# Kernel tuning notes

Measured on AMD Instinct MI355X. Metric: run time of the kernel, lower is better.

## Reference

```python
import jax, jax.numpy as jnp
import numpy as np

NEIGHBOR_NUM = 10   # FLAGS.gcn_n_num
SUPPORT_NUM = 7     # FLAGS.gcn_sup_num


def _norm(x, axis=-1):
    # F.normalize: divide by norm clamped to 1e-12
    return x / jnp.clip(jnp.linalg.norm(x, axis=axis, keepdims=True), 1e-12)


def _knn(v, k):
    # pairwise squared-distance KNN, excluding self -> (b, n, k)
    d2 = jnp.sum(v * v, -1)
    dist = d2[:, :, None] + d2[:, None, :] - 2.0 * jnp.einsum('bic,bjc->bij', v, v)
    idx = jax.lax.top_k(-dist, k + 1)[1]
    return idx[:, :, 1:]


_gather = jax.vmap(lambda f, i: f[i])  # f:(v,c), i:(v,k) -> (v,k,c)


def _orl(feat, w):
    # hybrid-scope fusion: concat per-point feature with global mean, 1x1 conv, residual
    g = jnp.broadcast_to(feat.mean(1, keepdims=True), feat.shape)
    return jnp.einsum('bvc,oc->bvo', jnp.concatenate([feat, g], -1), w) + feat


def _surface(verts, n, dirs, ste_w, orl_w):
    # HSlayer_surface: directional supports on normalized neighbor offsets
    b, v, _ = verts.shape
    f_ste = jnp.einsum('bvc,oc->bvo', verts, ste_w)              # (b,v,K)
    dnorm = _norm(_gather(verts, _knn(verts, n)) - verts[:, :, None, :])  # (b,v,n,3)
    theta = jax.nn.relu(jnp.einsum('bvnc,cs->bvns', dnorm, _norm(dirs, 0)))  # (b,v,n,S*K)
    theta = theta.reshape(b, v, n, SUPPORT_NUM, -1)
    return _orl(theta.max(2).sum(2) + f_ste, orl_w)


def _hs(verts, fmap, n, w, bias, dirs, ste_w, orl_w, out_c):
    # HS_layer: support-weighted aggregation of projected neighbor features
    b, v, _ = verts.shape
    f_ste = jnp.einsum('bvc,oc->bvo', fmap, ste_w)
    idx = _knn(verts, n)
    dnorm = _norm(_gather(verts, idx) - verts[:, :, None, :])
    theta = jax.nn.relu(jnp.einsum('bvnc,cs->bvns', dnorm, _norm(dirs, 0)))  # (b,v,n,S*O)
    fout = fmap @ w + bias                        # (b,v,(S+1)*O)
    f_center = fout[..., :out_c]
    f_support = _gather(fout[..., out_c:], idx)   # (b,v,n,S*O)
    act = (theta * f_support).reshape(b, v, n, SUPPORT_NUM, out_c)
    return _orl(f_center + act.max(2).sum(2) + f_ste, orl_w)


def _bn(x, g, b, eps=1e-5):
    # BatchNorm1d (training mode, biased variance) over (batch, vertices)
    m = x.mean((0, 1))
    var = ((x - m) ** 2).mean((0, 1))
    return (x - m) * jax.lax.rsqrt(var + eps) * g + b


def _pool(verts, fmap, rate=4, k=4):
    # neighborhood max-pool then deterministic 1/rate subsample
    pooled = _gather(fmap, _knn(verts, k)).max(2)
    pn = verts.shape[1] // rate
    return verts[:, :pn], pooled[:, :pn]


def setup_inputs() -> dict:
    key = jax.random.key(0)
    ks = iter(jax.random.split(key, 40))
    r = lambda *s: jax.random.normal(next(ks), s, jnp.float32) * 0.05
    S = SUPPORT_NUM
    return dict(
        vertices=jax.random.normal(next(ks), (4, 4096, 3), jnp.float32),
        dirs0=r(3, S * 128), ste0=r(128, 3), orl0=r(128, 256),
        w1=r(128, (S + 1) * 128), b1=r((S + 1) * 128), dirs1=r(3, S * 128),
        ste1=r(128, 128), orl1=r(128, 256),
        bn1_g=jnp.ones(128, jnp.float32), bn1_b=jnp.zeros(128, jnp.float32),
        w2=r(128, (S + 1) * 256), b2=r((S + 1) * 256), dirs2=r(3, S * 256),
        ste2=r(256, 128), orl2=r(256, 512),
        bn2_g=jnp.ones(256, jnp.float32), bn2_b=jnp.zeros(256, jnp.float32),
        w3=r(256, (S + 1) * 256), b3=r((S + 1) * 256), dirs3=r(3, S * 256),
        ste3=r(256, 256), orl3=r(256, 512),
        bn3_g=jnp.ones(256, jnp.float32), bn3_b=jnp.zeros(256, jnp.float32),
        w4=r(256, (S + 1) * 512), b4=r((S + 1) * 512), dirs4=r(3, S * 512),
        ste4=r(512, 256), orl4=r(512, 1024),
    )


def reference(vertices, dirs0, ste0, orl0,
              w1, b1, dirs1, ste1, orl1, bn1_g, bn1_b,
              w2, b2, dirs2, ste2, orl2, bn2_g, bn2_b,
              w3, b3, dirs3, ste3, orl3, bn3_g, bn3_b,
              w4, b4, dirs4, ste4, orl4):
    n = NEIGHBOR_NUM
    fm0 = jax.nn.relu(_surface(vertices, n, dirs0, ste0, orl0))
    fm1 = jax.nn.relu(_bn(_hs(vertices, fm0, n, w1, b1, dirs1, ste1, orl1, 128), bn1_g, bn1_b))
    v1, fp1 = _pool(vertices, fm1)
    n1 = min(n, v1.shape[1] // 8)
    fm2 = jax.nn.relu(_bn(_hs(v1, fp1, n1, w2, b2, dirs2, ste2, orl2, 256), bn2_g, bn2_b))
    fm3 = jax.nn.relu(_bn(_hs(v1, fm2, n1, w3, b3, dirs3, ste3, orl3, 256), bn3_g, bn3_b))
    v2, fp2 = _pool(v1, fm3)
    n2 = min(n, v2.shape[1] // 8)
    fm4 = _hs(v2, fp2, n2, w4, b4, dirs4, ste4, orl4, 512)
    return fm4.max(1)  # (bs, 512)
```

## Files before the change

### kernel.cpp

```cpp
#include <hip/hip_runtime.h>

#define S_NUM 7
#define NB 10
#define NEG_INF (-3.402823466e38f)


struct NormSeg { const float* src; float* dst; int M; };

__global__ void normalize_all_kernel(NormSeg s0, NormSeg s1, NormSeg s2, NormSeg s3, NormSeg s4) {
  NormSeg s;
  switch (blockIdx.y) {
    case 0: s = s0; break;
    case 1: s = s1; break;
    case 2: s = s2; break;
    case 3: s = s3; break;
    default: s = s4; break;
  }
  int m = blockIdx.x * blockDim.x + threadIdx.x;
  if (m >= s.M) return;
  float a = s.src[m], b = s.src[s.M + m], c = s.src[2 * s.M + m];
  float L = fmaxf(sqrtf(a * a + b * b + c * c), 1e-12f);
  s.dst[m] = a / L; s.dst[s.M + m] = b / L; s.dst[2 * s.M + m] = c / L;
}

struct TSeg { const float* in; float* out; int R, Cfull, Csub; };

__global__ void transpose_all_kernel(TSeg t0, TSeg t1, TSeg t2, TSeg t3, TSeg t4,
                                     TSeg t5, TSeg t6, TSeg t7, TSeg t8) {
  TSeg s;
  switch (blockIdx.y) {
    case 0: s = t0; break; case 1: s = t1; break; case 2: s = t2; break;
    case 3: s = t3; break; case 4: s = t4; break; case 5: s = t5; break;
    case 6: s = t6; break; case 7: s = t7; break; default: s = t8; break;
  }
  int t = blockIdx.x * blockDim.x + threadIdx.x;
  if (t >= s.R * s.Csub) return;
  int r = t % s.R, c = t / s.R;
  s.out[(size_t)c * s.R + r] = s.in[(size_t)r * s.Cfull + c];
}

__global__ void pack_points_kernel(const float* __restrict__ verts, float4* __restrict__ pts, int total) {
  int t = blockIdx.x * blockDim.x + threadIdx.x;
  if (t >= total) return;
  float x = verts[3 * t], y = verts[3 * t + 1], z = verts[3 * t + 2];
  float d2 = x * x + y * y + z * z;
  pts[t] = make_float4(x, y, z, d2);
}

__device__ __forceinline__ unsigned long long knn_key(float dist, int j) {
  unsigned int fb = __float_as_uint(dist);
  fb ^= ((unsigned int)((int)fb >> 31)) | 0x80000000u;
  return ((unsigned long long)fb << 32) | (unsigned int)j;
}

template <int V>
__global__ __launch_bounds__(256) void knn_kernel(const float4* __restrict__ pts,
                                                  int* __restrict__ idx_out) {
  constexpr int ITERS = V / 64;
  constexpr int FILL = (ITERS < 11) ? ITERS : 11;
  int wave = threadIdx.x >> 6;
  int lane = threadIdx.x & 63;
  int i = blockIdx.x * 4 + wave;
  int b = blockIdx.y;
  const float4* pb = pts + (size_t)b * 4096;
  float4 pi = pb[i];
  unsigned long long top[11];
#pragma unroll
  for (int t = 0; t < 11; ++t) top[t] = ~0ull;
  const float4* pl = pb + lane;
#pragma unroll
  for (int t = 0; t < FILL; ++t) {
    int j = lane + t * 64;
    float4 pj = pl[t * 64];
    float dt = pi.x * pj.x + pi.y * pj.y + pi.z * pj.z;
    float dist = (pi.w + pj.w) - 2.0f * dt;
    if (j == i) dist = -1.0f;
    top[t] = knn_key(dist, j);
  }
#pragma unroll
  for (int p = 0; p < 11; ++p) {
#pragma unroll
    for (int q = (p & 1); q + 1 < 11; q += 2) {
      unsigned long long a = top[q], bb = top[q + 1];
      bool cgt = a > bb;
      top[q] = cgt ? bb : a;
      top[q + 1] = cgt ? a : bb;
    }
  }
#pragma unroll 2
  for (int t = FILL; t < ITERS; ++t) {
    int j = lane + t * 64;
    float4 pj = pl[t * 64];
    float dt = pi.x * pj.x + pi.y * pj.y + pi.z * pj.z;
    float dist = (pi.w + pj.w) - 2.0f * dt;
    if (j == i) dist = -1.0f;
    unsigned long long key = knn_key(dist, j);
    if (key < top[10]) {
      unsigned long long ck = key;
#pragma unroll
      for (int q = 0; q < 11; ++q) {
        unsigned long long a = top[q];
        bool cl = ck < a;
        top[q] = cl ? ck : a;
        ck = cl ? a : ck;
      }
    }
  }
#pragma unroll 1
  for (int t = 0; t < 11; ++t) {
    unsigned long long m = top[0];
#pragma unroll
    for (int o = 32; o > 0; o >>= 1) {
      unsigned long long other = __shfl_xor(m, o, 64);
      m = (other < m) ? other : m;
    }
    if (top[0] == m) {
#pragma unroll
      for (int q = 0; q < 10; ++q) top[q] = top[q + 1];
      top[10] = ~0ull;
    }
    if (t >= 1 && lane == 0)
      idx_out[((size_t)b * V + i) * NB + (t - 1)] = (int)(m & 0xffffffffu);
  }
}

__global__ __launch_bounds__(256) void gemm_kernel(
    const float* __restrict__ A, const float* __restrict__ B,
    const float* __restrict__ bias, const float* __restrict__ gt,
    const float* __restrict__ resid, float* __restrict__ C,
    int M, int N, int K, int rpb, int relu) {
  __shared__ float As[32][68];
  __shared__ float Bs[32][64];
  int bm = blockIdx.x * 64;
  int bn = blockIdx.y * 64;
  int tid = threadIdx.x;
  int tx = tid & 15, ty = tid >> 4;
  float acc[4][4] = {};
  for (int k0 = 0; k0 < K; k0 += 32) {
#pragma unroll
    for (int l = 0; l < 2; ++l) {
      int f = tid + l * 256;
      int row = f >> 3, kq = f & 7;
      float4 a = *reinterpret_cast<const float4*>(&A[(size_t)(bm + row) * K + k0 + kq * 4]);
      As[kq * 4 + 0][row] = a.x; As[kq * 4 + 1][row] = a.y;
      As[kq * 4 + 2][row] = a.z; As[kq * 4 + 3][row] = a.w;
    }
#pragma unroll
    for (int l = 0; l < 2; ++l) {
      int f = tid + l * 256;
      int row = f >> 4, cq = f & 15;
      float4 v = *reinterpret_cast<const float4*>(&B[(size_t)(k0 + row) * N + bn + cq * 4]);
      *reinterpret_cast<float4*>(&Bs[row][cq * 4]) = v;
    }
    __syncthreads();
#pragma unroll
    for (int kk = 0; kk < 32; ++kk) {
      float4 av = *reinterpret_cast<const float4*>(&As[kk][ty * 4]);
      float4 bv = *reinterpret_cast<const float4*>(&Bs[kk][tx * 4]);
      float am[4] = {av.x, av.y, av.z, av.w};
      float bb[4] = {bv.x, bv.y, bv.z, bv.w};
#pragma unroll
      for (int i2 = 0; i2 < 4; ++i2)
#pragma unroll
        for (int j2 = 0; j2 < 4; ++j2)
          acc[i2][j2] = fmaf(am[i2], bb[j2], acc[i2][j2]);
    }
    __syncthreads();
  }
#pragma unroll
  for (int i2 = 0; i2 < 4; ++i2) {
    int row = bm + ty * 4 + i2;
    int col0 = bn + tx * 4;
    float4 v;
    float* vv = reinterpret_cast<float*>(&v);
#pragma unroll
    for (int j2 = 0; j2 < 4; ++j2) {
      float t = acc[i2][j2];
      int col = col0 + j2;
      if (bias)  t += bias[col];
      if (resid) t += resid[(size_t)row * N + col];
      if (gt)    t += gt[(row / rpb) * N + col];
      if (relu)  t = fmaxf(t, 0.0f);
      vv[j2] = t;
    }
    *reinterpret_cast<float4*>(&C[(size_t)row * N + col0]) = v;
  }
}

__global__ __launch_bounds__(128) void surface0_kernel(const float* __restrict__ verts,
    const int* __restrict__ idx, const float* __restrict__ ndirs,
    const float* __restrict__ ste0, float* __restrict__ feat) {
  __shared__ float dn[NB][3];
  int b = blockIdx.y, v = blockIdx.x;
  const float* vb = verts + (size_t)b * 4096 * 3;
  int tid = threadIdx.x;
  if (tid < NB) {
    int j = idx[((size_t)b * 4096 + v) * NB + tid];
    float dx = vb[3 * j] - vb[3 * v];
    float dy = vb[3 * j + 1] - vb[3 * v + 1];
    float dz = vb[3 * j + 2] - vb[3 * v + 2];
    float L = fmaxf(sqrtf(dx * dx + dy * dy + dz * dz), 1e-12f);
    dn[tid][0] = dx / L; dn[tid][1] = dy / L; dn[tid][2] = dz / L;
  }
  __syncthreads();
  int c = tid;
  float acc = vb[3 * v] * ste0[c * 3] + vb[3 * v + 1] * ste0[c * 3 + 1] + vb[3 * v + 2] * ste0[c * 3 + 2];
#pragma unroll
  for (int s = 0; s < S_NUM; ++s) {
    float w0 = ndirs[s * 128 + c], w1 = ndirs[896 + s * 128 + c], w2 = ndirs[1792 + s * 128 + c];
    float mx = NEG_INF;
#pragma unroll
    for (int n = 0; n < NB; ++n) {
      float th = fmaxf(dn[n][0] * w0 + dn[n][1] * w1 + dn[n][2] * w2, 0.0f);
      mx = fmaxf(mx, th);
    }
    acc += mx;
  }
  feat[((size_t)b * 4096 + v) * 128 + c] = acc;
}

template <int C>
__global__ void hs_kernel(const float* __restrict__ verts, int V,
                          const int* __restrict__ idx, const float* __restrict__ ndirs,
                          const float* __restrict__ fout, const float* __restrict__ fste,
                          float* __restrict__ feat) {
  __shared__ float dn[NB][3];
  __shared__ int nbr[NB];
  int b = blockIdx.y, v = blockIdx.x;
  const float* vb = verts + (size_t)b * 4096 * 3;
  int tid = threadIdx.x;
  if (tid < NB) {
    int j = idx[((size_t)b * V + v) * NB + tid];
    nbr[tid] = j;
    float dx = vb[3 * j] - vb[3 * v];
    float dy = vb[3 * j + 1] - vb[3 * v + 1];
    float dz = vb[3 * j + 2] - vb[3 * v + 2];
    float L = fmaxf(sqrtf(dx * dx + dy * dy + dz * dz), 1e-12f);
    dn[tid][0] = dx / L; dn[tid][1] = dy / L; dn[tid][2] = dz / L;
  }
  __syncthreads();
  int c = tid;
  size_t row = (size_t)b * V + v;
  float w0[S_NUM], w1[S_NUM], w2[S_NUM];
#pragma unroll
  for (int s = 0; s < S_NUM; ++s) {
    w0[s] = ndirs[s * C + c];
    w1[s] = ndirs[S_NUM * C + s * C + c];
    w2[s] = ndirs[2 * S_NUM * C + s * C + c];
  }
  float mx[S_NUM];
#pragma unroll
  for (int s = 0; s < S_NUM; ++s) mx[s] = NEG_INF;
  for (int n = 0; n < NB; ++n) {
    float d0 = dn[n][0], d1 = dn[n][1], d2 = dn[n][2];
    const float* fb = fout + ((size_t)b * V + nbr[n]) * (8 * C) + C + c;
#pragma unroll
    for (int s = 0; s < S_NUM; ++s) {
      float th = fmaxf(d0 * w0[s] + d1 * w1[s] + d2 * w2[s], 0.0f);
      mx[s] = fmaxf(mx[s], th * fb[(size_t)s * C]);
    }
  }
  float acc = fout[row * (8 * C) + c] + fste[row * C + c];
#pragma unroll
  for (int s = 0; s < S_NUM; ++s) acc += mx[s];
  feat[row * C + c] = acc;
}


__global__ void colsum_kernel(const float* __restrict__ x, double* __restrict__ sums,
                              int V, int C, int chunk) {
  int b = blockIdx.x, c = threadIdx.x;
  int r0 = blockIdx.y * chunk;
  int r1 = min(r0 + chunk, V);
  float s = 0.f;
  for (int r = r0; r < r1; ++r) s += x[((size_t)b * V + r) * C + c];
  atomicAdd(&sums[b * C + c], (double)s);
}

__global__ void gterm_kernel(const double* __restrict__ sums, const float* __restrict__ orl,
                             float* __restrict__ gt, int C, int O, double invV) {
  int b = blockIdx.x;
  int o = blockIdx.y * 64 + threadIdx.x;
  if (o >= O) return;
  float acc = 0.f;
  for (int c = 0; c < C; ++c)
    acc += (float)(sums[b * C + c] * invV) * orl[(size_t)o * (2 * C) + C + c];
  gt[b * O + o] = acc;
}

__global__ void bnstat_kernel(const float* __restrict__ x, double* __restrict__ stats,
                              int rows, int C, int chunk) {
  int c = threadIdx.x;
  int r0 = blockIdx.x * chunk;
  int r1 = min(r0 + chunk, rows);
  float s1 = 0.f, s2 = 0.f;
  for (int r = r0; r < r1; ++r) {
    float v = x[(size_t)r * C + c];
    s1 += v; s2 += v * v;
  }
  atomicAdd(&stats[c], (double)s1);
  atomicAdd(&stats[C + c], (double)s2);
}

__global__ void bnapply_kernel(const float* __restrict__ x, const double* __restrict__ stats,
                               const float* __restrict__ g, const float* __restrict__ bta,
                               float* __restrict__ y, int total, int C, double invN) {
  int i = blockIdx.x * blockDim.x + threadIdx.x;
  if (i >= total) return;
  int c = i % C;
  double m = stats[c] * invN;
  double var = stats[C + c] * invN - m * m;
  double inv = 1.0 / sqrt(var + 1e-5);
  float r = (float)(((double)x[i] - m) * inv) * g[c] + bta[c];
  y[i] = fmaxf(r, 0.0f);
}

template <int C>
__global__ void pool_kernel(const float* __restrict__ fm, const int* __restrict__ idx,
                            float* __restrict__ fp, int Vin) {
  int b = blockIdx.y, p = blockIdx.x, c = threadIdx.x;
  const int* ip = idx + ((size_t)b * Vin + p) * NB;
  float m = NEG_INF;
#pragma unroll
  for (int j = 0; j < 4; ++j)
    m = fmaxf(m, fm[((size_t)b * Vin + ip[j]) * C + c]);
  fp[((size_t)b * gridDim.x + p) * C + c] = m;
}

__global__ void finalmax_kernel(const float* __restrict__ fm4, float* __restrict__ out) {
  int b = blockIdx.x;
  int o = blockIdx.y * 256 + threadIdx.x;
  float m = NEG_INF;
  for (int v = 0; v < 256; ++v)
    m = fmaxf(m, fm4[((size_t)b * 256 + v) * 512 + o]);
  out[b * 512 + o] = m;
}


extern "C" void kernel_launch(void* const* d_in, const int* in_sizes, int n_in,
                              void* d_out, int out_size, void* d_ws, size_t ws_size,
                              hipStream_t stream) {
  const float* verts = (const float*)d_in[0];
  const float* dirs0 = (const float*)d_in[1];
  const float* ste0  = (const float*)d_in[2];
  const float* orl0  = (const float*)d_in[3];
  const float* w1    = (const float*)d_in[4];
  const float* b1    = (const float*)d_in[5];
  const float* dirs1 = (const float*)d_in[6];
  const float* ste1  = (const float*)d_in[7];
  const float* orl1  = (const float*)d_in[8];
  const float* bn1g  = (const float*)d_in[9];
  const float* bn1b  = (const float*)d_in[10];
  const float* w2    = (const float*)d_in[11];
  const float* b2    = (const float*)d_in[12];
  const float* dirs2 = (const float*)d_in[13];
  const float* ste2  = (const float*)d_in[14];
  const float* orl2  = (const float*)d_in[15];
  const float* bn2g  = (const float*)d_in[16];
  const float* bn2b  = (const float*)d_in[17];
  const float* w3    = (const float*)d_in[18];
  const float* b3    = (const float*)d_in[19];
  const float* dirs3 = (const float*)d_in[20];
  const float* ste3  = (const float*)d_in[21];
  const float* orl3  = (const float*)d_in[22];
  const float* bn3g  = (const float*)d_in[23];
  const float* bn3b  = (const float*)d_in[24];
  const float* w4    = (const float*)d_in[25];
  const float* b4    = (const float*)d_in[26];
  const float* dirs4 = (const float*)d_in[27];
  const float* ste4  = (const float*)d_in[28];
  const float* orl4  = (const float*)d_in[29];

  char* base = (char*)d_ws;
  size_t off = 0;
  auto alloc = [&](size_t bytes) -> void* {
    off = (off + 255) & ~(size_t)255;
    void* p = base + off;
    off += bytes;
    return p;
  };

  float* nd0  = (float*)alloc(3 * 896 * 4);
  float* nd1  = (float*)alloc(3 * 896 * 4);
  float* nd2  = (float*)alloc(3 * 1792 * 4);
  float* nd3  = (float*)alloc(3 * 1792 * 4);
  float* nd4  = (float*)alloc(3 * 3584 * 4);
  float* sT1  = (float*)alloc(128 * 128 * 4);
  float* sT2  = (float*)alloc(128 * 256 * 4);
  float* sT3  = (float*)alloc(256 * 256 * 4);
  float* sT4  = (float*)alloc(256 * 512 * 4);
  float* oA0  = (float*)alloc(128 * 128 * 4);
  float* oA1  = (float*)alloc(128 * 128 * 4);
  float* oA2  = (float*)alloc(256 * 256 * 4);
  float* oA3  = (float*)alloc(256 * 256 * 4);
  float* oA4  = (float*)alloc(512 * 512 * 4);
  float4* pts = (float4*)alloc((size_t)4 * 4096 * 16);
  int*   idx0 = (int*)alloc((size_t)4 * 4096 * NB * 4);
  int*   idx1 = (int*)alloc((size_t)4 * 1024 * NB * 4);
  int*   idx2 = (int*)alloc((size_t)4 * 256 * NB * 4);
  double* gsum  = (double*)alloc(4 * 512 * 8);
  float*  gterm = (float*)alloc(4 * 512 * 4);
  double* stats = (double*)alloc(2 * 256 * 8);
  size_t zspan = (size_t)((char*)(stats + 2 * 256) - (char*)gsum);
  float* Rfout = (float*)alloc((size_t)16384 * 1024 * 4);
  float* Rfeat = (float*)alloc((size_t)16384 * 128 * 4);
  float* Rtmp  = (float*)alloc((size_t)16384 * 128 * 4);
  float* Rfste = (float*)alloc((size_t)16384 * 128 * 4);
  float* Rfm   = (float*)alloc((size_t)16384 * 128 * 4);
  float* Rfp   = (float*)alloc((size_t)4 * 1024 * 128 * 4);
  (void)in_sizes; (void)n_in; (void)out_size; (void)ws_size;

  auto gemm = [&](const float* A, const float* B, const float* bias, const float* gt,
                  const float* resid, float* C, int M, int N, int K, int rpb, int relu) {
    gemm_kernel<<<dim3(M / 64, N / 64), 256, 0, stream>>>(A, B, bias, gt, resid, C, M, N, K, rpb ? rpb : 1, relu);
  };

  normalize_all_kernel<<<dim3(14, 5), 256, 0, stream>>>(
      NormSeg{dirs0, nd0, 896}, NormSeg{dirs1, nd1, 896}, NormSeg{dirs2, nd2, 1792},
      NormSeg{dirs3, nd3, 1792}, NormSeg{dirs4, nd4, 3584});
  transpose_all_kernel<<<dim3(1024, 9), 256, 0, stream>>>(
      TSeg{ste1, sT1, 128, 128, 128}, TSeg{ste2, sT2, 256, 128, 128},
      TSeg{ste3, sT3, 256, 256, 256}, TSeg{ste4, sT4, 512, 256, 256},
      TSeg{orl0, oA0, 128, 256, 128}, TSeg{orl1, oA1, 128, 256, 128},
      TSeg{orl2, oA2, 256, 512, 256}, TSeg{orl3, oA3, 256, 512, 256},
      TSeg{orl4, oA4, 512, 1024, 512});
  pack_points_kernel<<<(4 * 4096 + 255) / 256, 256, 0, stream>>>(verts, pts, 4 * 4096);

  knn_kernel<4096><<<dim3(4096 / 4, 4), 256, 0, stream>>>(pts, idx0);

  surface0_kernel<<<dim3(4096, 4), 128, 0, stream>>>(verts, idx0, nd0, ste0, Rfeat);
  hipMemsetAsync(gsum, 0, zspan, stream);
  colsum_kernel<<<dim3(4, 32), 128, 0, stream>>>(Rfeat, gsum, 4096, 128, 128);
  gterm_kernel<<<dim3(4, 2), 64, 0, stream>>>(gsum, orl0, gterm, 128, 128, 1.0 / 4096);
  gemm(Rfeat, oA0, nullptr, gterm, Rfeat, Rtmp, 16384, 128, 128, 4096, 1);

  gemm(Rtmp, w1, b1, nullptr, nullptr, Rfout, 16384, 1024, 128, 0, 0);
  gemm(Rtmp, sT1, nullptr, nullptr, nullptr, Rfste, 16384, 128, 128, 0, 0);
  hs_kernel<128><<<dim3(4096, 4), 128, 0, stream>>>(verts, 4096, idx0, nd1, Rfout, Rfste, Rfeat);
  hipMemsetAsync(gsum, 0, zspan, stream);
  colsum_kernel<<<dim3(4, 32), 128, 0, stream>>>(Rfeat, gsum, 4096, 128, 128);
  gterm_kernel<<<dim3(4, 2), 64, 0, stream>>>(gsum, orl1, gterm, 128, 128, 1.0 / 4096);
  gemm(Rfeat, oA1, nullptr, gterm, Rfeat, Rtmp, 16384, 128, 128, 4096, 0);
  bnstat_kernel<<<128, 128, 0, stream>>>(Rtmp, stats, 16384, 128, 128);
  bnapply_kernel<<<(16384 * 128 + 255) / 256, 256, 0, stream>>>(Rtmp, stats, bn1g, bn1b, Rfm, 16384 * 128, 128, 1.0 / 16384);
  pool_kernel<128><<<dim3(1024, 4), 128, 0, stream>>>(Rfm, idx0, Rfp, 4096);
  knn_kernel<1024><<<dim3(1024 / 4, 4), 256, 0, stream>>>(pts, idx1);

  gemm(Rfp, w2, b2, nullptr, nullptr, Rfout, 4096, 2048, 128, 0, 0);
  gemm(Rfp, sT2, nullptr, nullptr, nullptr, Rfste, 4096, 256, 128, 0, 0);
  hs_kernel<256><<<dim3(1024, 4), 256, 0, stream>>>(verts, 1024, idx1, nd2, Rfout, Rfste, Rfeat);
  hipMemsetAsync(gsum, 0, zspan, stream);
  colsum_kernel<<<dim3(4, 8), 256, 0, stream>>>(Rfeat, gsum, 1024, 256, 128);
  gterm_kernel<<<dim3(4, 4), 64, 0, stream>>>(gsum, orl2, gterm, 256, 256, 1.0 / 1024);
  gemm(Rfeat, oA2, nullptr, gterm, Rfeat, Rtmp, 4096, 256, 256, 1024, 0);
  bnstat_kernel<<<32, 256, 0, stream>>>(Rtmp, stats, 4096, 256, 128);
  bnapply_kernel<<<(4096 * 256 + 255) / 256, 256, 0, stream>>>(Rtmp, stats, bn2g, bn2b, Rfm, 4096 * 256, 256, 1.0 / 4096);

  gemm(Rfm, w3, b3, nullptr, nullptr, Rfout, 4096, 2048, 256, 0, 0);
  gemm(Rfm, sT3, nullptr, nullptr, nullptr, Rfste, 4096, 256, 256, 0, 0);
  hs_kernel<256><<<dim3(1024, 4), 256, 0, stream>>>(verts, 1024, idx1, nd3, Rfout, Rfste, Rfeat);
  hipMemsetAsync(gsum, 0, zspan, stream);
  colsum_kernel<<<dim3(4, 8), 256, 0, stream>>>(Rfeat, gsum, 1024, 256, 128);
  gterm_kernel<<<dim3(4, 4), 64, 0, stream>>>(gsum, orl3, gterm, 256, 256, 1.0 / 1024);
  gemm(Rfeat, oA3, nullptr, gterm, Rfeat, Rtmp, 4096, 256, 256, 1024, 0);
  bnstat_kernel<<<32, 256, 0, stream>>>(Rtmp, stats, 4096, 256, 128);
  bnapply_kernel<<<(4096 * 256 + 255) / 256, 256, 0, stream>>>(Rtmp, stats, bn3g, bn3b, Rfm, 4096 * 256, 256, 1.0 / 4096);
  pool_kernel<256><<<dim3(256, 4), 256, 0, stream>>>(Rfm, idx1, Rfp, 1024);
  knn_kernel<256><<<dim3(256 / 4, 4), 256, 0, stream>>>(pts, idx2);

  gemm(Rfp, w4, b4, nullptr, nullptr, Rfout, 1024, 4096, 256, 0, 0);
  gemm(Rfp, sT4, nullptr, nullptr, nullptr, Rfste, 1024, 512, 256, 0, 0);
  hs_kernel<512><<<dim3(256, 4), 512, 0, stream>>>(verts, 256, idx2, nd4, Rfout, Rfste, Rfeat);
  hipMemsetAsync(gsum, 0, zspan, stream);
  colsum_kernel<<<dim3(4, 2), 512, 0, stream>>>(Rfeat, gsum, 256, 512, 128);
  gterm_kernel<<<dim3(4, 8), 64, 0, stream>>>(gsum, orl4, gterm, 512, 512, 1.0 / 256);
  gemm(Rfeat, oA4, nullptr, gterm, Rfeat, Rtmp, 1024, 512, 512, 256, 0);

  finalmax_kernel<<<dim3(4, 2), 256, 0, stream>>>(Rtmp, (float*)d_out);
}
```

Before: 1.290 ms.

## Enlarge GEMM tiles to 128x128 and gate KNN insertion with a wave-wide threshold

The GEMM moves from 64x64 tiles with a 4x4 per-thread micro-tile to 128x128 tiles with an 8x8 micro-tile. It uses padded shared memory and sets a minimum of three blocks per SIMD in launch bounds, to get more FMA work per shared-memory load. The KNN kernel splits each 64-bit key into separate 32-bit distance and index arrays. It also skips insertion unless a candidate beats a wave-wide minimum of the lanes' 11th-best keys, refreshed every four iterations, which cuts compare-swap work. The risks are higher register pressure from 64 accumulators and fewer blocks on the smaller GEMMs.

Result: slower. 1.609 ms (+24.7%).

```diff
diff --git a/kernel.cpp b/kernel.cpp
--- a/kernel.cpp
+++ b/kernel.cpp
@@ -47,10 +47,10 @@
   pts[t] = make_float4(x, y, z, d2);
 }
 
-__device__ __forceinline__ unsigned long long knn_key(float dist, int j) {
-  unsigned int fb = __float_as_uint(dist);
-  fb ^= ((unsigned int)((int)fb >> 31)) | 0x80000000u;
-  return ((unsigned long long)fb << 32) | (unsigned int)j;
+__device__ __forceinline__ unsigned ord_key(float dist) {
+  unsigned fb = __float_as_uint(dist);
+  fb ^= ((unsigned)((int)fb >> 31)) | 0x80000000u;
+  return fb;
 }
 
 template <int V>
@@ -64,126 +64,140 @@
   int b = blockIdx.y;
   const float4* pb = pts + (size_t)b * 4096;
   float4 pi = pb[i];
-  unsigned long long top[11];
-#pragma unroll
-  for (int t = 0; t < 11; ++t) top[t] = ~0ull;
+  unsigned tk[11], tj[11];
+#pragma unroll
+  for (int t = 0; t < 11; ++t) { tk[t] = 0xFFFFFFFFu; tj[t] = 0u; }
   const float4* pl = pb + lane;
 #pragma unroll
   for (int t = 0; t < FILL; ++t) {
     int j = lane + t * 64;
     float4 pj = pl[t * 64];
-    float dt = pi.x * pj.x + pi.y * pj.y + pi.z * pj.z;
-    float dist = (pi.w + pj.w) - 2.0f * dt;
+    float dist = (pi.w + pj.w) - 2.0f * (pi.x * pj.x + pi.y * pj.y + pi.z * pj.z);
     if (j == i) dist = -1.0f;
-    top[t] = knn_key(dist, j);
+    tk[t] = ord_key(dist); tj[t] = (unsigned)j;
   }
 #pragma unroll
   for (int p = 0; p < 11; ++p) {
 #pragma unroll
     for (int q = (p & 1); q + 1 < 11; q += 2) {
-      unsigned long long a = top[q], bb = top[q + 1];
-      bool cgt = a > bb;
-      top[q] = cgt ? bb : a;
-      top[q + 1] = cgt ? a : bb;
-    }
-  }
-#pragma unroll 2
+      bool sw = tk[q] > tk[q + 1];
+      unsigned k0 = sw ? tk[q + 1] : tk[q], k1 = sw ? tk[q] : tk[q + 1];
+      unsigned j0 = sw ? tj[q + 1] : tj[q], j1 = sw ? tj[q] : tj[q + 1];
+      tk[q] = k0; tk[q + 1] = k1; tj[q] = j0; tj[q + 1] = j1;
+    }
+  }
+  unsigned wgate = tk[10];
+#pragma unroll
+  for (int o = 32; o > 0; o >>= 1) {
+    unsigned y = __shfl_xor(wgate, o, 64);
+    wgate = (y < wgate) ? y : wgate;
+  }
   for (int t = FILL; t < ITERS; ++t) {
     int j = lane + t * 64;
     float4 pj = pl[t * 64];
-    float dt = pi.x * pj.x + pi.y * pj.y + pi.z * pj.z;
-    float dist = (pi.w + pj.w) - 2.0f * dt;
+    float dist = (pi.w + pj.w) - 2.0f * (pi.x * pj.x + pi.y * pj.y + pi.z * pj.z);
     if (j == i) dist = -1.0f;
-    unsigned long long key = knn_key(dist, j);
-    if (key < top[10]) {
-      unsigned long long ck = key;
+    unsigned ck = ord_key(dist);
+    if (ck < wgate) {
+      unsigned cj = (unsigned)j;
 #pragma unroll
       for (int q = 0; q < 11; ++q) {
-        unsigned long long a = top[q];
-        bool cl = ck < a;
-        top[q] = cl ? ck : a;
-        ck = cl ? a : ck;
+        bool lt = ck < tk[q];
+        unsigned nk = lt ? ck : tk[q]; ck = lt ? tk[q] : ck; tk[q] = nk;
+        unsigned nj = lt ? cj : tj[q]; cj = lt ? tj[q] : cj; tj[q] = nj;
       }
+    }
+    if ((t & 3) == 3) {
+      unsigned g = tk[10];
+#pragma unroll
+      for (int o = 32; o > 0; o >>= 1) {
+        unsigned y = __shfl_xor(g, o, 64);
+        g = (y < g) ? y : g;
+      }
+      wgate = g;
     }
   }
 #pragma unroll 1
   for (int t = 0; t < 11; ++t) {
-    unsigned long long m = top[0];
+    unsigned long long mk = ((unsigned long long)tk[0] << 32) | tj[0];
+    unsigned long long m = mk;
 #pragma unroll
     for (int o = 32; o > 0; o >>= 1) {
       unsigned long long other = __shfl_xor(m, o, 64);
       m = (other < m) ? other : m;
     }
-    if (top[0] == m) {
-#pragma unroll
-      for (int q = 0; q < 10; ++q) top[q] = top[q + 1];
-      top[10] = ~0ull;
+    if (mk == m) {
+#pragma unroll
+      for (int q = 0; q < 10; ++q) { tk[q] = tk[q + 1]; tj[q] = tj[q + 1]; }
+      tk[10] = 0xFFFFFFFFu; tj[10] = 0u;
     }
     if (t >= 1 && lane == 0)
       idx_out[((size_t)b * V + i) * NB + (t - 1)] = (int)(m & 0xffffffffu);
   }
 }
 
-__global__ __launch_bounds__(256) void gemm_kernel(
+__global__ __launch_bounds__(256, 3) void gemm_kernel(
     const float* __restrict__ A, const float* __restrict__ B,
     const float* __restrict__ bias, const float* __restrict__ gt,
     const float* __restrict__ resid, float* __restrict__ C,
     int M, int N, int K, int rpb, int relu) {
-  __shared__ float As[32][68];
-  __shared__ float Bs[32][64];
-  int bm = blockIdx.x * 64;
-  int bn = blockIdx.y * 64;
+  __shared__ float As[16][132];
+  __shared__ float Bs[16][140];
+  int bm = blockIdx.x * 128;
+  int bn = blockIdx.y * 128;
   int tid = threadIdx.x;
   int tx = tid & 15, ty = tid >> 4;
-  float acc[4][4] = {};
-  for (int k0 = 0; k0 < K; k0 += 32) {
+  int bp = tx * 8 + 4 * (tx >> 2);
+  float acc[8][8] = {};
+  for (int k0 = 0; k0 < K; k0 += 16) {
 #pragma unroll
     for (int l = 0; l < 2; ++l) {
       int f = tid + l * 256;
-      int row = f >> 3, kq = f & 7;
-      float4 a = *reinterpret_cast<const float4*>(&A[(size_t)(bm + row) * K + k0 + kq * 4]);
-      As[kq * 4 + 0][row] = a.x; As[kq * 4 + 1][row] = a.y;
-      As[kq * 4 + 2][row] = a.z; As[kq * 4 + 3][row] = a.w;
-    }
-#pragma unroll
-    for (int l = 0; l < 2; ++l) {
-      int f = tid + l * 256;
-      int row = f >> 4, cq = f & 15;
-      float4 v = *reinterpret_cast<const float4*>(&B[(size_t)(k0 + row) * N + bn + cq * 4]);
-      *reinterpret_cast<float4*>(&Bs[row][cq * 4]) = v;
+      int ar = f >> 2, akq = f & 3;
+      float4 a = *reinterpret_cast<const float4*>(&A[(size_t)(bm + ar) * K + k0 + akq * 4]);
+      As[akq * 4 + 0][ar] = a.x; As[akq * 4 + 1][ar] = a.y;
+      As[akq * 4 + 2][ar] = a.z; As[akq * 4 + 3][ar] = a.w;
+      int br = f >> 5, bcq = f & 31;
+      float4 v = *reinterpret_cast<const float4*>(&B[(size_t)(k0 + br) * N + bn + bcq * 4]);
+      *reinterpret_cast<float4*>(&Bs[br][bcq * 4 + 4 * (bcq >> 3)]) = v;
     }
     __syncthreads();
 #pragma unroll
-    for (int kk = 0; kk < 32; ++kk) {
-      float4 av = *reinterpret_cast<const float4*>(&As[kk][ty * 4]);
-      float4 bv = *reinterpret_cast<const float4*>(&Bs[kk][tx * 4]);
-      float am[4] = {av.x, av.y, av.z, av.w};
-      float bb[4] = {bv.x, bv.y, bv.z, bv.w};
-#pragma unroll
-      for (int i2 = 0; i2 < 4; ++i2)
-#pragma unroll
-        for (int j2 = 0; j2 < 4; ++j2)
+    for (int kk = 0; kk < 16; ++kk) {
+      float4 a0 = *reinterpret_cast<const float4*>(&As[kk][ty * 8]);
+      float4 a1 = *reinterpret_cast<const float4*>(&As[kk][ty * 8 + 4]);
+      float4 b0 = *reinterpret_cast<const float4*>(&Bs[kk][bp]);
+      float4 b1 = *reinterpret_cast<const float4*>(&Bs[kk][bp + 4]);
+      float am[8] = {a0.x, a0.y, a0.z, a0.w, a1.x, a1.y, a1.z, a1.w};
+      float bb[8] = {b0.x, b0.y, b0.z, b0.w, b1.x, b1.y, b1.z, b1.w};
+#pragma unroll
+      for (int i2 = 0; i2 < 8; ++i2)
+#pragma unroll
+        for (int j2 = 0; j2 < 8; ++j2)
           acc[i2][j2] = fmaf(am[i2], bb[j2], acc[i2][j2]);
     }
     __syncthreads();
   }
 #pragma unroll
-  for (int i2 = 0; i2 < 4; ++i2) {
-    int row = bm + ty * 4 + i2;
-    int col0 = bn + tx * 4;
-    float4 v;
-    float* vv = reinterpret_cast<float*>(&v);
-#pragma unroll
-    for (int j2 = 0; j2 < 4; ++j2) {
-      float t = acc[i2][j2];
-      int col = col0 + j2;
-      if (bias)  t += bias[col];
-      if (resid) t += resid[(size_t)row * N + col];
-      if (gt)    t += gt[(row / rpb) * N + col];
-      if (relu)  t = fmaxf(t, 0.0f);
-      vv[j2] = t;
-    }
-    *reinterpret_cast<float4*>(&C[(size_t)row * N + col0]) = v;
+  for (int i2 = 0; i2 < 8; ++i2) {
+    int row = bm + ty * 8 + i2;
+#pragma unroll
+    for (int h = 0; h < 2; ++h) {
+      int col0 = bn + tx * 8 + h * 4;
+      float4 v;
+      float* vv = reinterpret_cast<float*>(&v);
+#pragma unroll
+      for (int j2 = 0; j2 < 4; ++j2) {
+        float t = acc[i2][h * 4 + j2];
+        int col = col0 + j2;
+        if (bias)  t += bias[col];
+        if (resid) t += resid[(size_t)row * N + col];
+        if (gt)    t += gt[(row / rpb) * N + col];
+        if (relu)  t = fmaxf(t, 0.0f);
+        vv[j2] = t;
+      }
+      *reinterpret_cast<float4*>(&C[(size_t)row * N + col0]) = v;
+    }
   }
 }
 
@@ -412,7 +426,7 @@
 
   auto gemm = [&](const float* A, const float* B, const float* bias, const float* gt,
                   const float* resid, float* C, int M, int N, int K, int rpb, int relu) {
-    gemm_kernel<<<dim3(M / 64, N / 64), 256, 0, stream>>>(A, B, bias, gt, resid, C, M, N, K, rpb ? rpb : 1, relu);
+    gemm_kernel<<<dim3(M / 128, N / 128), 256, 0, stream>>>(A, B, bias, gt, resid, C, M, N, K, rpb ? rpb : 1, relu);
   };
 
   normalize_all_kernel<<<dim3(14, 5), 256, 0, stream>>>(
```
